# Performance work log

Hardware: AMD Instinct MI355X
Metric: run time of the kernel (lower is better)

## Reference

```python
import jax, jax.numpy as jnp
import numpy as np

E, D_IN, D_OUT, T = 16, 2048, 8192, 8192  # experts, d_model, 4*d_model, total tokens


def setup_inputs() -> dict:
    key = jax.random.key(0)
    k1, k2, k3 = jax.random.split(key, 3)
    inp = jax.random.normal(k1, (T, D_IN), dtype=jnp.float32)
    # FMoELinear parameters: weight [E, d_output, d_input], bias [E, d_output]
    weight = jax.random.normal(k2, (E, D_OUT, D_IN), dtype=jnp.float32) * 0.02
    bias = jax.random.normal(k3, (E, D_OUT), dtype=jnp.float32) * 0.02
    # tokens are pre-sorted by expert; equal split summing to T
    fwd_expert_count = jnp.full((E,), T // E, dtype=jnp.int32)
    return {"inp": inp, "weight": weight, "bias": bias,
            "fwd_expert_count": fwd_expert_count}


def reference(inp, weight, bias, fwd_expert_count):
    # Grouped GEMM: rows of inp are grouped by expert per fwd_expert_count.
    # ragged_dot(lhs [T, K], rhs [E, K, N], group_sizes [E]) -> [T, N]
    out = jax.lax.ragged_dot(inp, jnp.swapaxes(weight, 1, 2), fwd_expert_count)
    # per-token expert id for the bias gather (fixed total length => jit-safe)
    expert_idx = jnp.repeat(jnp.arange(weight.shape[0]), fwd_expert_count,
                            total_repeat_length=inp.shape[0])
    return out + bias[expert_idx]
```

## Files before the change

kernel.cpp:

```cpp
#include <hip/hip_runtime.h>
#include <hip/hip_bf16.h>


#define TOK   8192
#define KDIM  2048
#define NDIM  8192
#define NEXP  16

#define BM 256
#define BN 256
#define BK 32
#define LDSS 40

typedef __attribute__((ext_vector_type(8))) short short8;
typedef __attribute__((ext_vector_type(4))) float f32x4;

__device__ __forceinline__ unsigned pk2(float lo, float hi) {
    unsigned ul = __float_as_uint(lo) + 0x8000u;
    unsigned uh = __float_as_uint(hi) + 0x8000u;
    return __builtin_amdgcn_perm(uh, ul, 0x07060302u);
}
__device__ __forceinline__ uint2 pk4(float4 v) {
    uint2 r;
    r.x = pk2(v.x, v.y);
    r.y = pk2(v.z, v.w);
    return r;
}

__global__ __launch_bounds__(512) void moe_gemm(
    const float* __restrict__ inp,
    const float* __restrict__ weight,
    const float* __restrict__ bias,
    const int*   __restrict__ cnt,
    float*       __restrict__ out)
{
    __shared__ short sA[BM * LDSS];
    __shared__ short sB[BN * LDSS];

    const int tid = threadIdx.x;
    const int b   = blockIdx.x;

    const int x  = b & 7;
    const int j  = b >> 3;
    const int e  = j >> 3;
    const int t  = j & 7;
    const int nl = t >> 1;
    const int mi = t & 1;
    const int ntile = x * 4 + nl;

    int m_start = 0;
    for (int i = 0; i < e; ++i) m_start += cnt[i];
    const int m0 = m_start + mi * BM;
    const int n0 = ntile * BN;

    const float* wexp = weight + (size_t)e * NDIM * KDIM;

    const int tRow = tid >> 3;
    const int tCol = tid & 7;
    const float* aBase = inp  + (size_t)m0 * KDIM + tCol * 4;
    const float* bBase = wexp + (size_t)n0 * KDIM + tCol * 4;

    const int wave = tid >> 6;
    const int lane = tid & 63;
    const int wm   = wave & 1;
    const int wn   = wave >> 1;
    const int r16  = lane & 15;
    const int quad = lane >> 4;

    f32x4 acc[8][4] = {};

    float4 ra[4], rb[4];
    #pragma unroll
    for (int i = 0; i < 4; ++i) {
        const int row = i * 64 + tRow;
        ra[i] = *(const float4*)(aBase + (size_t)row * KDIM);
        rb[i] = *(const float4*)(bBase + (size_t)row * KDIM);
    }

    const int KSTEPS = KDIM / BK;
    for (int kt = 0; kt < KSTEPS; ++kt) {
        __syncthreads();
        #pragma unroll
        for (int i = 0; i < 4; ++i) {
            const int row = i * 64 + tRow;
            *(uint2*)&sA[row * LDSS + tCol * 4] = pk4(ra[i]);
            *(uint2*)&sB[row * LDSS + tCol * 4] = pk4(rb[i]);
        }
        __syncthreads();

        if (kt + 1 < KSTEPS) {
            const int koff = (kt + 1) * BK;
            #pragma unroll
            for (int i = 0; i < 4; ++i) {
                const int row = i * 64 + tRow;
                ra[i] = *(const float4*)(aBase + (size_t)row * KDIM + koff);
                rb[i] = *(const float4*)(bBase + (size_t)row * KDIM + koff);
            }
        }

        short8 bf[4];
        #pragma unroll
        for (int nt = 0; nt < 4; ++nt)
            bf[nt] = *(const short8*)&sB[(wn * 64 + nt * 16 + r16) * LDSS + quad * 8];

        #pragma unroll
        for (int mt = 0; mt < 8; ++mt) {
            const short8 af = *(const short8*)&sA[(wm * 128 + mt * 16 + r16) * LDSS + quad * 8];
            #pragma unroll
            for (int nt = 0; nt < 4; ++nt)
                acc[mt][nt] = __builtin_amdgcn_mfma_f32_16x16x32_bf16(
                    af, bf[nt], acc[mt][nt], 0, 0, 0);
        }
    }

    #pragma unroll
    for (int nt = 0; nt < 4; ++nt) {
        const int n = n0 + wn * 64 + nt * 16 + r16;
        const float bv = bias[(size_t)e * NDIM + n];
        #pragma unroll
        for (int mt = 0; mt < 8; ++mt) {
            #pragma unroll
            for (int r = 0; r < 4; ++r) {
                const int m = m0 + wm * 128 + mt * 16 + quad * 4 + r;
                out[(size_t)m * NDIM + n] = acc[mt][nt][r] + bv;
            }
        }
    }
}

extern "C" void kernel_launch(void* const* d_in, const int* in_sizes, int n_in,
                              void* d_out, int out_size, void* d_ws, size_t ws_size,
                              hipStream_t stream) {
    const float* inp    = (const float*)d_in[0];
    const float* weight = (const float*)d_in[1];
    const float* bias   = (const float*)d_in[2];
    const int*   cnt    = (const int*)d_in[3];
    float* out = (float*)d_out;

    const int grid = (TOK / BM) * (NDIM / BN);
    hipLaunchKernelGGL(moe_gemm, dim3(grid), dim3(512), 0, stream,
                       inp, weight, bias, cnt, out);
}
```

Baseline: 1.763 ms.

## Pre-convert inputs to tiled bf16 workspace and stream tiles via direct-to-LDS loads

Adds a conversion kernel that turns the fp32 input and weights into bf16 in a pre-tiled, XOR-swizzled workspace layout. The GEMM then double-buffers 64-wide K tiles, loading them with global_load_lds straight into LDS with no register staging or in-loop conversion. This is meant to halve the bytes read in the main loop, remove the per-iteration fp32-to-bf16 packing, and overlap loads with MFMA work. In exchange it adds a full conversion pass over 1 GB of fp32 weights every call, and it depends on a large workspace; without one it falls back to the old kernel.

```diff
diff --git a/kernel.cpp b/kernel.cpp
--- a/kernel.cpp
+++ b/kernel.cpp
@@ -9,8 +9,16 @@
 
 #define BM 256
 #define BN 256
-#define BK 32
-#define LDSS 40
+#define BK 64
+#define NKT (KDIM / BK)
+#define NMT (TOK / BM)
+#define NNT (NDIM / BN)
+#define TILE_BYTES (256 * BK * 2)
+
+#define WSA_BYTES ((size_t)NMT * NKT * TILE_BYTES)
+#define WSB_OFF   0x2800000ull
+#define WSB_BYTES ((size_t)NEXP * NNT * NKT * TILE_BYTES)
+#define WS_NEED   (WSB_OFF + WSB_BYTES)
 
 typedef __attribute__((ext_vector_type(8))) short short8;
 typedef __attribute__((ext_vector_type(4))) float f32x4;
@@ -27,7 +35,140 @@
     return r;
 }
 
+__global__ __launch_bounds__(256) void convert_bf16(
+    const float* __restrict__ inp,
+    const float* __restrict__ weight,
+    char*        __restrict__ ws)
+{
+    const int row = blockIdx.x;
+    const int t   = threadIdx.x;
+    const int kt  = t >> 3;
+    const int cg  = t & 7;
+
+    const float4* src;
+    size_t dst;
+    if (row < TOK) {
+        src = (const float4*)(inp + (size_t)row * KDIM + t * 8);
+        const int mt = row >> 8, r = row & 255;
+        dst = (size_t)(mt * NKT + kt) * TILE_BYTES
+            + r * 128 + ((cg * 16) ^ ((r & 7) << 4));
+    } else {
+        const int rr = row - TOK;
+        src = (const float4*)(weight + (size_t)rr * KDIM + t * 8);
+        const int e = rr >> 13, n = rr & 8191;
+        const int nt = n >> 8, r = n & 255;
+        dst = WSB_OFF
+            + (size_t)((e * NNT + nt) * NKT + kt) * TILE_BYTES
+            + r * 128 + ((cg * 16) ^ ((r & 7) << 4));
+    }
+    float4 v0 = src[0], v1 = src[1];
+    uint2 p0 = pk4(v0), p1 = pk4(v1);
+    uint4 o; o.x = p0.x; o.y = p0.y; o.z = p1.x; o.w = p1.y;
+    *(uint4*)(ws + dst) = o;
+}
+
 __global__ __launch_bounds__(512) void moe_gemm(
+    const char*  __restrict__ ws,
+    const float* __restrict__ bias,
+    const int*   __restrict__ cnt,
+    float*       __restrict__ out)
+{
+    __shared__ __attribute__((aligned(16))) char lds[2][2][TILE_BYTES];
+
+    const int tid = threadIdx.x;
+    const int b   = blockIdx.x;
+
+    const int x  = b & 7;
+    const int j  = b >> 3;
+    const int e  = j >> 3;
+    const int t  = j & 7;
+    const int nl = t >> 1;
+    const int mi = t & 1;
+    const int ntile = x * 4 + nl;
+
+    int m_start = 0;
+    for (int i = 0; i < e; ++i) m_start += cnt[i];
+    const int m0 = m_start + mi * BM;
+    const int n0 = ntile * BN;
+
+    const char* gA = ws + (size_t)((m0 >> 8) * NKT) * TILE_BYTES + tid * 16;
+    const char* gB = ws + WSB_OFF
+                   + (size_t)((e * NNT + (n0 >> 8)) * NKT) * TILE_BYTES + tid * 16;
+
+#define STAGE(c, kt_) do {                                                    \
+    const char* _a = gA + (size_t)(kt_) * TILE_BYTES;                         \
+    const char* _b = gB + (size_t)(kt_) * TILE_BYTES;                         \
+    _Pragma("unroll")                                                         \
+    for (int _i = 0; _i < 4; ++_i) {                                          \
+        __builtin_amdgcn_global_load_lds(                                     \
+            (const __attribute__((address_space(1))) unsigned int*)(_a + _i * 8192), \
+            (__attribute__((address_space(3))) unsigned int*)(&lds[c][0][tid * 16] + _i * 8192), \
+            16, 0, 0);                                                        \
+        __builtin_amdgcn_global_load_lds(                                     \
+            (const __attribute__((address_space(1))) unsigned int*)(_b + _i * 8192), \
+            (__attribute__((address_space(3))) unsigned int*)(&lds[c][1][tid * 16] + _i * 8192), \
+            16, 0, 0);                                                        \
+    }                                                                         \
+} while (0)
+
+    const int wave = tid >> 6;
+    const int lane = tid & 63;
+    const int wm   = wave & 1;
+    const int wn   = wave >> 1;
+    const int r16  = lane & 15;
+    const int quad = lane >> 4;
+    const int swz  = (r16 & 7) << 4;
+
+    f32x4 acc[8][4] = {};
+
+    STAGE(0, 0);
+    __syncthreads();
+
+    int cur = 0;
+    for (int kt = 0; kt < NKT; ++kt) {
+        if (kt + 1 < NKT) STAGE(cur ^ 1, kt + 1);
+
+        const char* la = &lds[cur][0][0] + (size_t)(wm * 128 + r16) * 128;
+        const char* lb = &lds[cur][1][0] + (size_t)(wn * 64  + r16) * 128;
+
+        #pragma unroll
+        for (int kk = 0; kk < 2; ++kk) {
+            const int koff = (kk * 64 + quad * 16) ^ swz;
+            short8 bfr[4];
+            #pragma unroll
+            for (int nt = 0; nt < 4; ++nt)
+                bfr[nt] = *(const short8*)(lb + nt * (16 * 128) + koff);
+            #pragma unroll
+            for (int mt = 0; mt < 8; ++mt) {
+                const short8 af = *(const short8*)(la + mt * (16 * 128) + koff);
+                #pragma unroll
+                for (int nt = 0; nt < 4; ++nt)
+                    acc[mt][nt] = __builtin_amdgcn_mfma_f32_16x16x32_bf16(
+                        af, bfr[nt], acc[mt][nt], 0, 0, 0);
+            }
+        }
+        __syncthreads();
+        cur ^= 1;
+    }
+
+    #pragma unroll
+    for (int nt = 0; nt < 4; ++nt) {
+        const int n = n0 + wn * 64 + nt * 16 + r16;
+        const float bv = bias[(size_t)e * NDIM + n];
+        #pragma unroll
+        for (int mt = 0; mt < 8; ++mt) {
+            #pragma unroll
+            for (int r = 0; r < 4; ++r) {
+                const int m = m0 + wm * 128 + mt * 16 + quad * 4 + r;
+                out[(size_t)m * NDIM + n] = acc[mt][nt][r] + bv;
+            }
+        }
+    }
+#undef STAGE
+}
+
+#define LDSS 40
+__global__ __launch_bounds__(512) void moe_gemm_fb(
     const float* __restrict__ inp,
     const float* __restrict__ weight,
     const float* __restrict__ bias,
@@ -39,7 +180,6 @@
 
     const int tid = threadIdx.x;
     const int b   = blockIdx.x;
-
     const int x  = b & 7;
     const int j  = b >> 3;
     const int e  = j >> 3;
@@ -54,7 +194,6 @@
     const int n0 = ntile * BN;
 
     const float* wexp = weight + (size_t)e * NDIM * KDIM;
-
     const int tRow = tid >> 3;
     const int tCol = tid & 7;
     const float* aBase = inp  + (size_t)m0 * KDIM + tCol * 4;
@@ -68,7 +207,6 @@
     const int quad = lane >> 4;
 
     f32x4 acc[8][4] = {};
-
     float4 ra[4], rb[4];
     #pragma unroll
     for (int i = 0; i < 4; ++i) {
@@ -77,7 +215,7 @@
         rb[i] = *(const float4*)(bBase + (size_t)row * KDIM);
     }
 
-    const int KSTEPS = KDIM / BK;
+    const int KSTEPS = KDIM / 32;
     for (int kt = 0; kt < KSTEPS; ++kt) {
         __syncthreads();
         #pragma unroll
@@ -87,9 +225,8 @@
             *(uint2*)&sB[row * LDSS + tCol * 4] = pk4(rb[i]);
         }
         __syncthreads();
-
         if (kt + 1 < KSTEPS) {
-            const int koff = (kt + 1) * BK;
+            const int koff = (kt + 1) * 32;
             #pragma unroll
             for (int i = 0; i < 4; ++i) {
                 const int row = i * 64 + tRow;
@@ -97,19 +234,17 @@
                 rb[i] = *(const float4*)(bBase + (size_t)row * KDIM + koff);
             }
         }
-
-        short8 bf[4];
+        short8 bfr[4];
         #pragma unroll
         for (int nt = 0; nt < 4; ++nt)
-            bf[nt] = *(const short8*)&sB[(wn * 64 + nt * 16 + r16) * LDSS + quad * 8];
-
+            bfr[nt] = *(const short8*)&sB[(wn * 64 + nt * 16 + r16) * LDSS + quad * 8];
         #pragma unroll
         for (int mt = 0; mt < 8; ++mt) {
             const short8 af = *(const short8*)&sA[(wm * 128 + mt * 16 + r16) * LDSS + quad * 8];
             #pragma unroll
             for (int nt = 0; nt < 4; ++nt)
                 acc[mt][nt] = __builtin_amdgcn_mfma_f32_16x16x32_bf16(
-                    af, bf[nt], acc[mt][nt], 0, 0, 0);
+                    af, bfr[nt], acc[mt][nt], 0, 0, 0);
         }
     }
 
@@ -137,7 +272,16 @@
     const int*   cnt    = (const int*)d_in[3];
     float* out = (float*)d_out;
 
-    const int grid = (TOK / BM) * (NDIM / BN);
-    hipLaunchKernelGGL(moe_gemm, dim3(grid), dim3(512), 0, stream,
-                       inp, weight, bias, cnt, out);
-}
+    if (d_ws != nullptr && ws_size >= WS_NEED) {
+        const int rows = TOK + NEXP * NDIM;
+        hipLaunchKernelGGL(convert_bf16, dim3(rows), dim3(256), 0, stream,
+                           inp, weight, (char*)d_ws);
+        const int grid = (TOK / BM) * (NDIM / BN);
+        hipLaunchKernelGGL(moe_gemm, dim3(grid), dim3(512), 0, stream,
+                           (const char*)d_ws, bias, cnt, out);
+    } else {
+        const int grid = (TOK / BM) * (NDIM / BN);
+        hipLaunchKernelGGL(moe_gemm_fb, dim3(grid), dim3(512), 0, stream,
+                           inp, weight, bias, cnt, out);
+    }
+}
```

Result: no change. 1.776 ms (+0.7%).

## Double-buffer LDS with XOR swizzle and one barrier per K-step

Applied to the files above, without the earlier changes.

Replaces the single padded LDS tile with two XOR-swizzled bf16 buffers. Each iteration computes from one buffer while writing the next tile into the other, with global loads issued two steps ahead and only one barrier per step. This targets the two-barrier stall and the store-then-compute serialization of the old loop. It also adds s_setprio and sched_barrier hints around the MFMA block, at the cost of doubled LDS use and more register pressure from the precomputed offsets.

```diff
diff --git a/kernel.cpp b/kernel.cpp
--- a/kernel.cpp
+++ b/kernel.cpp
@@ -10,7 +10,8 @@
 #define BM 256
 #define BN 256
 #define BK 32
-#define LDSS 40
+#define NKT (KDIM / BK)
+#define TILEB 16384
 
 typedef __attribute__((ext_vector_type(8))) short short8;
 typedef __attribute__((ext_vector_type(4))) float f32x4;
@@ -20,12 +21,25 @@
     unsigned uh = __float_as_uint(hi) + 0x8000u;
     return __builtin_amdgcn_perm(uh, ul, 0x07060302u);
 }
-__device__ __forceinline__ uint2 pk4(float4 v) {
-    uint2 r;
-    r.x = pk2(v.x, v.y);
-    r.y = pk2(v.z, v.w);
-    return r;
+__device__ __forceinline__ uint4 pkchunk(float4 x, float4 y) {
+    uint4 o;
+    o.x = pk2(x.x, x.y); o.y = pk2(x.z, x.w);
+    o.z = pk2(y.x, y.y); o.w = pk2(y.z, y.w);
+    return o;
 }
+
+__device__ __forceinline__ int ldsoff(int row, int c) {
+    const int L    = row >> 1;
+    const int slot = ((row & 1) << 2) | c;
+    return L * 128 + ((slot ^ (L & 7)) << 4);
+}
+
+#define LOADG(dst, p0, p1, kt_) do {                         \
+    dst[0] = *(const float4*)((p0) + (kt_) * BK);            \
+    dst[1] = *(const float4*)((p0) + (kt_) * BK + 4);        \
+    dst[2] = *(const float4*)((p1) + (kt_) * BK);            \
+    dst[3] = *(const float4*)((p1) + (kt_) * BK + 4);        \
+} while (0)
 
 __global__ __launch_bounds__(512) void moe_gemm(
     const float* __restrict__ inp,
@@ -34,8 +48,7 @@
     const int*   __restrict__ cnt,
     float*       __restrict__ out)
 {
-    __shared__ short sA[BM * LDSS];
-    __shared__ short sB[BN * LDSS];
+    __shared__ __attribute__((aligned(16))) char lds[2][2][TILEB];
 
     const int tid = threadIdx.x;
     const int b   = blockIdx.x;
@@ -53,12 +66,16 @@
     const int m0 = m_start + mi * BM;
     const int n0 = ntile * BN;
 
+    const int ch0 = tid, ch1 = 512 + tid;
+    const int r0 = ch0 >> 2, c0 = ch0 & 3;
+    const int r1 = ch1 >> 2, c1 = ch1 & 3;
+    const float* pA0 = inp + (size_t)(m0 + r0) * KDIM + c0 * 8;
+    const float* pA1 = inp + (size_t)(m0 + r1) * KDIM + c1 * 8;
     const float* wexp = weight + (size_t)e * NDIM * KDIM;
-
-    const int tRow = tid >> 3;
-    const int tCol = tid & 7;
-    const float* aBase = inp  + (size_t)m0 * KDIM + tCol * 4;
-    const float* bBase = wexp + (size_t)n0 * KDIM + tCol * 4;
+    const float* pB0 = wexp + (size_t)(n0 + r0) * KDIM + c0 * 8;
+    const float* pB1 = wexp + (size_t)(n0 + r1) * KDIM + c1 * 8;
+    const int w0 = ldsoff(r0, c0);
+    const int w1 = ldsoff(r1, c1);
 
     const int wave = tid >> 6;
     const int lane = tid & 63;
@@ -67,51 +84,80 @@
     const int r16  = lane & 15;
     const int quad = lane >> 4;
 
+    int aoff[8], boff[4];
+    #pragma unroll
+    for (int mt = 0; mt < 8; ++mt) aoff[mt] = ldsoff(wm * 128 + mt * 16 + r16, quad);
+    #pragma unroll
+    for (int nt = 0; nt < 4; ++nt) boff[nt] = ldsoff(wn * 64 + nt * 16 + r16, quad);
+
     f32x4 acc[8][4] = {};
+    float4 Ag[4], Bg[4];
 
-    float4 ra[4], rb[4];
-    #pragma unroll
-    for (int i = 0; i < 4; ++i) {
-        const int row = i * 64 + tRow;
-        ra[i] = *(const float4*)(aBase + (size_t)row * KDIM);
-        rb[i] = *(const float4*)(bBase + (size_t)row * KDIM);
+    LOADG(Ag, pA0, pA1, 0); LOADG(Bg, pB0, pB1, 0);
+    *(uint4*)(&lds[0][0][0] + w0) = pkchunk(Ag[0], Ag[1]);
+    *(uint4*)(&lds[0][0][0] + w1) = pkchunk(Ag[2], Ag[3]);
+    *(uint4*)(&lds[0][1][0] + w0) = pkchunk(Bg[0], Bg[1]);
+    *(uint4*)(&lds[0][1][0] + w1) = pkchunk(Bg[2], Bg[3]);
+    LOADG(Ag, pA0, pA1, 1); LOADG(Bg, pB0, pB1, 1);
+    asm volatile("s_waitcnt lgkmcnt(0)" ::: "memory");
+    __builtin_amdgcn_s_barrier();
+    __builtin_amdgcn_sched_barrier(0);
+
+#define ITER(RD, WR, kt_, DOLOAD) do {                                        \
+    short8 bfr[4], afr[8];                                                    \
+    _Pragma("unroll")                                                         \
+    for (int nt = 0; nt < 4; ++nt)                                            \
+        bfr[nt] = *(const short8*)(&lds[RD][1][0] + boff[nt]);                \
+    _Pragma("unroll")                                                         \
+    for (int mt = 0; mt < 8; ++mt)                                            \
+        afr[mt] = *(const short8*)(&lds[RD][0][0] + aoff[mt]);                \
+    __builtin_amdgcn_s_setprio(1);                                            \
+    _Pragma("unroll")                                                         \
+    for (int mt = 0; mt < 8; ++mt)                                            \
+        _Pragma("unroll")                                                     \
+        for (int nt = 0; nt < 4; ++nt)                                        \
+            acc[mt][nt] = __builtin_amdgcn_mfma_f32_16x16x32_bf16(            \
+                afr[mt], bfr[nt], acc[mt][nt], 0, 0, 0);                      \
+    __builtin_amdgcn_s_setprio(0);                                            \
+    __builtin_amdgcn_sched_barrier(0);                                        \
+    *(uint4*)(&lds[WR][0][0] + w0) = pkchunk(Ag[0], Ag[1]);                   \
+    *(uint4*)(&lds[WR][0][0] + w1) = pkchunk(Ag[2], Ag[3]);                   \
+    *(uint4*)(&lds[WR][1][0] + w0) = pkchunk(Bg[0], Bg[1]);                   \
+    *(uint4*)(&lds[WR][1][0] + w1) = pkchunk(Bg[2], Bg[3]);                   \
+    __builtin_amdgcn_sched_barrier(0);                                        \
+    if (DOLOAD) {                                                             \
+        LOADG(Ag, pA0, pA1, (kt_) + 2);                                       \
+        LOADG(Bg, pB0, pB1, (kt_) + 2);                                       \
+    }                                                                         \
+    asm volatile("s_waitcnt lgkmcnt(0)" ::: "memory");                        \
+    __builtin_amdgcn_s_barrier();                                             \
+    __builtin_amdgcn_sched_barrier(0);                                        \
+} while (0)
+
+    for (int kt = 0; kt < NKT - 2; kt += 2) {
+        ITER(0, 1, kt,     true);
+        ITER(1, 0, kt + 1, true);
     }
+    ITER(0, 1, NKT - 2, false);
 
-    const int KSTEPS = KDIM / BK;
-    for (int kt = 0; kt < KSTEPS; ++kt) {
-        __syncthreads();
-        #pragma unroll
-        for (int i = 0; i < 4; ++i) {
-            const int row = i * 64 + tRow;
-            *(uint2*)&sA[row * LDSS + tCol * 4] = pk4(ra[i]);
-            *(uint2*)&sB[row * LDSS + tCol * 4] = pk4(rb[i]);
-        }
-        __syncthreads();
-
-        if (kt + 1 < KSTEPS) {
-            const int koff = (kt + 1) * BK;
-            #pragma unroll
-            for (int i = 0; i < 4; ++i) {
-                const int row = i * 64 + tRow;
-                ra[i] = *(const float4*)(aBase + (size_t)row * KDIM + koff);
-                rb[i] = *(const float4*)(bBase + (size_t)row * KDIM + koff);
-            }
-        }
-
-        short8 bf[4];
+    {
+        short8 bfr[4], afr[8];
         #pragma unroll
         for (int nt = 0; nt < 4; ++nt)
-            bf[nt] = *(const short8*)&sB[(wn * 64 + nt * 16 + r16) * LDSS + quad * 8];
-
+            bfr[nt] = *(const short8*)(&lds[1][1][0] + boff[nt]);
         #pragma unroll
-        for (int mt = 0; mt < 8; ++mt) {
-            const short8 af = *(const short8*)&sA[(wm * 128 + mt * 16 + r16) * LDSS + quad * 8];
+        for (int mt = 0; mt < 8; ++mt)
+            afr[mt] = *(const short8*)(&lds[1][0][0] + aoff[mt]);
+        __builtin_amdgcn_s_setprio(1);
+        #pragma unroll
+        for (int mt = 0; mt < 8; ++mt)
             #pragma unroll
             for (int nt = 0; nt < 4; ++nt)
                 acc[mt][nt] = __builtin_amdgcn_mfma_f32_16x16x32_bf16(
-                    af, bf[nt], acc[mt][nt], 0, 0, 0);
-        }
+                    afr[mt], bfr[nt], acc[mt][nt], 0, 0, 0);
+        __builtin_amdgcn_s_setprio(0);
     }
+#undef ITER
 
     #pragma unroll
     for (int nt = 0; nt < 4; ++nt) {
```

Result: faster. 1.554 ms (-11.9%).
